# Optimization experiments

Measured on AMD Instinct MI355X. Metric: run time of the kernel, lower is better.

Reference implementation:

```python
import math
import jax, jax.numpy as jnp
import numpy as np

jax.config.update("jax_enable_x64", True)

NUM_HEADS = 4
D_INNER = 256
D_STATE = 256
HEADDIM = D_INNER // NUM_HEADS
NUM_GRAPHS = 8
L_NODES = 512
N_NODES = NUM_GRAPHS * L_NODES
N_EDGES = 65536
TOL = 0.05  # self.tol


def dag_inverse(A, n):
    # Doubling Neumann series: (I+A)(I+A^2)(I+A^4)... = sum_{k<2^ceil(log2 n)} A^k
    # equals (I - A)^{-1} when A is nilpotent (DAG with diameter <= n).
    j = 2 ** math.ceil(math.log2(n))
    I = jnp.eye(A.shape[-1], dtype=A.dtype)
    last = A
    out = I + A
    for _ in range(2, int(math.log2(j)) + 1):
        last = last @ last
        out = out @ (I + last)
    return out


def _forward(x, Bmat, Cmat, dt, dt_edge, dt_bias, D, edge_index, data_batch, diameter):
    Bg, L, H, Hd = NUM_GRAPHS, L_NODES, NUM_HEADS, HEADDIM
    N = x.shape[0]
    # nodes are sorted by graph with equal graph sizes -> local index within graph
    local = jnp.arange(N) - data_batch * L

    def to_dense(v):  # (N, ...) -> (Bg, L, ...), equivalent of to_dense_batch
        return jnp.zeros((Bg, L) + v.shape[1:], v.dtype).at[data_batch, local].set(v)

    x_r = to_dense(x).reshape(Bg, L, H, Hd).transpose(0, 2, 1, 3)  # b n l h
    B_b = jnp.broadcast_to(to_dense(Bmat)[:, None], (Bg, H, L, D_STATE))  # broadcast_bc_in_heads
    C_b = jnp.broadcast_to(to_dense(Cmat)[:, None], (Bg, H, L, D_STATE))

    dt3 = dt.reshape(N, H, 4).transpose(2, 1, 0)  # 'l (n c) -> c n l'
    dt_self_d = to_dense(dt3[3].T).transpose(0, 2, 1)  # (b, n, l)

    def mul_dt_A(d):
        # A_log is a zeros buffer (with_A=False) -> A = -exp(0) = -1
        return -jax.nn.softplus(d + dt_bias[None, :, None])

    dt_A_node = mul_dt_A(dt3[:3])  # (3, n, N)
    dt_A_edge = mul_dt_A(dt_edge.reshape(-1, H, 1).transpose(2, 1, 0))  # (1, n, E)

    src, dst = edge_index[0], edge_index[1]
    dt_A = (dt_A_node[0][:, src] + dt_A_node[1][:, dst] + dt_A_edge[0]) / 3.0  # (n, E)
    vals = jnp.exp(dt_A).T  # (E, n)
    # to_dense_adj: scatter-add edge attrs into dense (b, l1, l2, n)
    adj = jnp.zeros((Bg, L, L, H), vals.dtype).at[
        data_batch[src], local[src], local[dst]].add(vals)
    adj = adj.transpose(0, 3, 1, 2)  # (b, n, l1, l2)

    dt_dummy = to_dense(jnp.exp(dt_A_node[2]).T).transpose(0, 2, 1)  # (b, n, l)
    # normalize_mat('sum_leq', sub_constraint='max')
    normalizer = jnp.maximum(1.0, adj.sum(-1) + dt_dummy)
    A_mat = adj / (normalizer[..., None] + TOL)

    # I_minus_A: fp64 doubling inverse of (I - A^T)
    Lm = dag_inverse(jnp.swapaxes(A_mat.astype(jnp.float64), -1, -2), diameter)
    Lm = Lm.astype(x.dtype)
    L_norm = Lm * dt_self_d[:, :, None, :]  # L * dt_self.unsqueeze(-2)

    y = jnp.einsum('bnld,bnlt,bntd,bnth->bnlh', C_b, L_norm, B_b, x_r)
    y = y + x_r * D[None, :, None, None]
    y = y.transpose(0, 2, 3, 1).reshape(Bg, L, Hd * H)  # 'b n l h -> b l (h n)'
    return y.reshape(N, Hd * H)  # mask is all-True (equal-size graphs)


def setup_inputs():
    key = jax.random.key(0)
    ks = jax.random.split(key, 8)
    x = jax.random.normal(ks[0], (N_NODES, D_INNER), dtype=jnp.float32)
    Bmat = jax.random.normal(ks[1], (N_NODES, D_STATE), dtype=jnp.float32)
    Cmat = jax.random.normal(ks[2], (N_NODES, D_STATE), dtype=jnp.float32)
    dt = jax.random.normal(ks[3], (N_NODES, NUM_HEADS * 4), dtype=jnp.float32)
    dt_edge = jax.random.normal(ks[4], (N_EDGES, NUM_HEADS), dtype=jnp.float32)
    per_graph = N_EDGES // NUM_GRAPHS
    g = jnp.repeat(jnp.arange(NUM_GRAPHS), per_graph)
    src = g * L_NODES + jax.random.randint(ks[5], (N_EDGES,), 0, L_NODES)
    dst = g * L_NODES + jax.random.randint(ks[6], (N_EDGES,), 0, L_NODES)
    edge_index = jnp.stack([src, dst]).astype(jnp.int32)
    data_batch = jnp.repeat(jnp.arange(NUM_GRAPHS), L_NODES).astype(jnp.int32)
    # dt_bias init as in module __init__
    dt_min, dt_max = 1e-3, 1e-1
    u = jax.random.uniform(ks[7], (NUM_HEADS,))
    dtv = jnp.exp(u * (math.log(dt_max) - math.log(dt_min)) + math.log(dt_min))
    dtv = jnp.clip(dtv, 1e-4, None)
    dt_bias = (dtv + jnp.log(-jnp.expm1(-dtv))).astype(jnp.float32)
    D = jnp.ones((NUM_HEADS,), dtype=jnp.float32)
    return {"x": x, "Bmat": Bmat, "Cmat": Cmat, "dt": dt, "dt_edge": dt_edge,
            "dt_bias": dt_bias, "D": D, "edge_index": edge_index,
            "data_batch": data_batch, "diameter": 32}


def reference(x, Bmat, Cmat, dt, dt_edge, dt_bias, D, edge_index, data_batch, diameter):
    return _forward(x, Bmat, Cmat, dt, dt_edge, dt_bias, D, edge_index, data_batch, diameter)
```

## Files before the change

### kernel.cpp

```cpp
#include <hip/hip_runtime.h>
#include <math.h>

#define N_EDGES 65536
#define LNODE 512
#define DSTATE 256
#define DINNER 256
#define HEADD 64

using bf16x8 = __attribute__((ext_vector_type(8))) short;
using f32x4  = __attribute__((ext_vector_type(4))) float;
using us4    = __attribute__((ext_vector_type(4))) unsigned short;
using us8    = __attribute__((ext_vector_type(8))) unsigned short;

__device__ __forceinline__ float softplusf(float z) {
  return (z > 0.0f) ? (z + log1pf(expf(-z))) : log1pf(expf(z));
}
__device__ __forceinline__ float bf2f(unsigned short u) {
  unsigned int x = ((unsigned int)u) << 16;
  return __builtin_bit_cast(float, x);
}
__device__ __forceinline__ unsigned short f2bf(float f) {
  unsigned int x = __builtin_bit_cast(unsigned int, f);
  x += 0x7fffu + ((x >> 16) & 1u);
  return (unsigned short)(x >> 16);
}

__global__ __launch_bounds__(256) void zero_ws_kernel(float* __restrict__ G,
                                                      float* __restrict__ colsum) {
  const size_t i = (size_t)blockIdx.x * 256 + threadIdx.x;
  const float4 z = make_float4(0.0f, 0.0f, 0.0f, 0.0f);
  if (i < 2097152) {
    ((float4*)G)[i] = z;
  } else {
    ((float4*)colsum)[i - 2097152] = z;
  }
}

__global__ void scatter_edges_kernel(const float* __restrict__ dt,
                                     const float* __restrict__ dt_edge,
                                     const float* __restrict__ dt_bias,
                                     const int* __restrict__ edge_index,
                                     float* __restrict__ G,
                                     float* __restrict__ colsum) {
  int t = blockIdx.x * blockDim.x + threadIdx.x;
  if (t >= N_EDGES * 4) return;
  int e = t >> 2;
  int n = t & 3;
  int src = edge_index[e];
  int dst = edge_index[N_EDGES + e];
  float bias = dt_bias[n];
  float z0 = dt[src * 16 + n * 4 + 0] + bias;
  float z1 = dt[dst * 16 + n * 4 + 1] + bias;
  float z2 = dt_edge[e * 4 + n] + bias;
  float val = expf(-(softplusf(z0) + softplusf(z1) + softplusf(z2)) * (1.0f / 3.0f));
  int b = src >> 9;
  int l1 = src & 511;
  int l2 = dst & 511;
  int bn = b * 4 + n;
  atomicAdd(&G[(((size_t)bn) << 18) + ((size_t)l2 << 9) + l1], val);
  atomicAdd(&colsum[bn * 512 + l1], val);
}

__global__ __launch_bounds__(256) void conv_kernel(const float* __restrict__ G,
                                                   const float* __restrict__ colsum,
                                                   const float* __restrict__ dt,
                                                   const float* __restrict__ dt_bias,
                                                   unsigned short* __restrict__ Prm,
                                                   unsigned short* __restrict__ Pt,
                                                   unsigned short* __restrict__ Q) {
  const int bn = blockIdx.y;
  const int n = bn & 3, b = bn >> 2;
  const size_t base = (size_t)bn << 18;
  const int tile = blockIdx.x;
  const int ro = (tile >> 4) << 5;
  const int co = (tile & 15) << 5;
  __shared__ float lds[32][33];
  __shared__ float sinv[32];
  const int t = threadIdx.x;
  if (t < 32) {
    const int col = co + t;
    float ssum = colsum[bn * 512 + col];
    float bias = dt_bias[n];
    float dummy = expf(-softplusf(dt[(size_t)(b * 512 + col) * 16 + n * 4 + 2] + bias));
    float norm = fmaxf(1.0f, ssum + dummy);
    sinv[t] = 1.0f / (norm + 0.05f);
  }
  __syncthreads();
  const int tr = t >> 3;
  const int tc0 = (t & 7) << 2;
  float4 gv = *(const float4*)(G + base + (size_t)(ro + tr) * 512 + co + tc0);
  float vv[4] = {gv.x, gv.y, gv.z, gv.w};
  us4 p, q;
#pragma unroll
  for (int j = 0; j < 4; ++j) {
    vv[j] *= sinv[tc0 + j];
    p[j] = f2bf(vv[j]);
    float qq = vv[j] + (((ro + tr) == (co + tc0 + j)) ? 1.0f : 0.0f);
    q[j] = f2bf(qq);
    lds[tc0 + j][tr] = vv[j];
  }
  *(us4*)(Prm + base + (size_t)(ro + tr) * 512 + co + tc0) = p;
  *(us4*)(Q + base + (size_t)(ro + tr) * 512 + co + tc0) = q;
  __syncthreads();
  us4 pt;
#pragma unroll
  for (int j = 0; j < 4; ++j) pt[j] = f2bf(lds[tr][tc0 + j]);
  *(us4*)(Pt + base + (size_t)(co + tr) * 512 + ro + tc0) = pt;
}

__global__ __launch_bounds__(256) void gemm_pair_kernel(
    const unsigned short* __restrict__ A0, const unsigned short* __restrict__ B0,
    unsigned short* __restrict__ C0rm, unsigned short* __restrict__ C0t,
    const unsigned short* __restrict__ Q0,
    const unsigned short* __restrict__ A1, const unsigned short* __restrict__ B1,
    unsigned short* __restrict__ C1rm, unsigned short* __restrict__ C1t,
    const unsigned short* __restrict__ Q1) {
  const int f = (blockIdx.z * gridDim.y + blockIdx.y) * gridDim.x + blockIdx.x;
  const int rres = f & 7;
  const int q = f >> 3;
  const int tile = q & 15;
  const int kk_ = ((q >> 4) << 3) + rres;
  const int bn = kk_ & 31;
  const int z = kk_ >> 5;

  const unsigned short* A    = z ? A1 : A0;
  const unsigned short* Bt   = z ? B1 : B0;
  unsigned short* Crm        = z ? C1rm : C0rm;
  unsigned short* Ct         = z ? C1t : C0t;
  const unsigned short* Qadd = z ? Q1 : Q0;

  const size_t off = (size_t)bn << 18;
  A += off; Bt += off;
  if (Crm) Crm += off;
  if (Ct) Ct += off;
  if (Qadd) Qadd += off;
  const int m0 = (tile >> 2) << 7;
  const int n0 = (tile & 3) << 7;
  __shared__ __align__(16) char lds[34816];
  const int tid = threadIdx.x;
  const int lane = tid & 63;
  const int w = tid >> 6;
  const int wr = w >> 1, wc = w & 1;

  f32x4 acc[4][4];
#pragma unroll
  for (int i = 0; i < 4; ++i)
#pragma unroll
    for (int j = 0; j < 4; ++j) acc[i][j] = (f32x4)(0.0f);

  auto stage = [&](int buf, int k0) {
    char* la = lds + buf * 16384;
    char* lb = la + 8192;
#pragma unroll
    for (int s = 0; s < 2; ++s) {
      const int fid = s * 256 + tid;
      const int r = fid >> 2;
      const int qs = (fid & 3) ^ ((r >> 1) & 3);
      const unsigned short* ga = A + (size_t)(m0 + r) * 512 + k0 + qs * 8;
      __builtin_amdgcn_global_load_lds(
          (const __attribute__((address_space(1))) void*)ga,
          (__attribute__((address_space(3))) void*)(la + s * 4096 + w * 1024 + (lane << 4)),
          16, 0, 0);
      const unsigned short* gb = Bt + (size_t)(n0 + r) * 512 + k0 + qs * 8;
      __builtin_amdgcn_global_load_lds(
          (const __attribute__((address_space(1))) void*)gb,
          (__attribute__((address_space(3))) void*)(lb + s * 4096 + w * 1024 + (lane << 4)),
          16, 0, 0);
    }
  };

  stage(0, 0);

#pragma unroll
  for (int t = 0; t < 16; ++t) {
    const int cur = t & 1;
    if (t < 15) {
      stage(cur ^ 1, (t + 1) * 32);
      asm volatile("s_waitcnt vmcnt(4)" ::: "memory");
    } else {
      asm volatile("s_waitcnt vmcnt(0)" ::: "memory");
    }
    __builtin_amdgcn_s_barrier();
    __builtin_amdgcn_sched_barrier(0);
    char* la = lds + cur * 16384;
    char* lb = la + 8192;
    const int gk = lane >> 4;
    bf16x8 av[4], bv[4];
#pragma unroll
    for (int mi = 0; mi < 4; ++mi) {
      const int r = wr * 64 + mi * 16 + (lane & 15);
      av[mi] = *(const bf16x8*)(la + r * 64 + ((gk ^ ((r >> 1) & 3)) << 4));
    }
#pragma unroll
    for (int ni = 0; ni < 4; ++ni) {
      const int r = wc * 64 + ni * 16 + (lane & 15);
      bv[ni] = *(const bf16x8*)(lb + r * 64 + ((gk ^ ((r >> 1) & 3)) << 4));
    }
#pragma unroll
    for (int mi = 0; mi < 4; ++mi)
#pragma unroll
      for (int ni = 0; ni < 4; ++ni)
        acc[mi][ni] = __builtin_amdgcn_mfma_f32_16x16x32_bf16(av[mi], bv[ni], acc[mi][ni], 0, 0, 0);
    __builtin_amdgcn_sched_barrier(0);
    __builtin_amdgcn_s_barrier();
  }

  const int cl = lane & 15;
  const int rg = (lane >> 4) << 2;
  unsigned short* tl = (unsigned short*)lds;
#pragma unroll
  for (int mi = 0; mi < 4; ++mi) {
#pragma unroll
    for (int ni = 0; ni < 4; ++ni) {
      const int lrow = wr * 64 + mi * 16 + rg;
      const int lcol = wc * 64 + ni * 16 + cl;
      const int gr = m0 + lrow;
      const int gc = n0 + lcol;
      float v0 = acc[mi][ni][0], v1 = acc[mi][ni][1];
      float v2 = acc[mi][ni][2], v3 = acc[mi][ni][3];
      if (Qadd) {
        v0 += bf2f(Qadd[(size_t)(gr + 0) * 512 + gc]);
        v1 += bf2f(Qadd[(size_t)(gr + 1) * 512 + gc]);
        v2 += bf2f(Qadd[(size_t)(gr + 2) * 512 + gc]);
        v3 += bf2f(Qadd[(size_t)(gr + 3) * 512 + gc]);
      }
      unsigned short h0 = f2bf(v0), h1 = f2bf(v1), h2 = f2bf(v2), h3 = f2bf(v3);
      if (Crm) {
        Crm[(size_t)(gr + 0) * 512 + gc] = h0;
        Crm[(size_t)(gr + 1) * 512 + gc] = h1;
        Crm[(size_t)(gr + 2) * 512 + gc] = h2;
        Crm[(size_t)(gr + 3) * 512 + gc] = h3;
      }
      if (Ct) {
        tl[lcol * 136 + lrow + 0] = h0;
        tl[lcol * 136 + lrow + 1] = h1;
        tl[lcol * 136 + lrow + 2] = h2;
        tl[lcol * 136 + lrow + 3] = h3;
      }
    }
  }
  if (Ct) {
    __syncthreads();
    const int c = tid >> 1;
    const int rh = (tid & 1) << 6;
    const unsigned short* srcp = tl + c * 136 + rh;
    unsigned short* dstp = Ct + (size_t)(n0 + c) * 512 + m0 + rh;
#pragma unroll
    for (int u = 0; u < 8; ++u)
      *(us8*)(dstp + u * 8) = *(const us8*)(srcp + u * 8);
  }
}

__global__ __launch_bounds__(256) void gemm_nt_kernel(const float* __restrict__ Cm,
                                                      const float* __restrict__ Bm,
                                                      float* __restrict__ S) {
  const int f = blockIdx.y * gridDim.x + blockIdx.x;
  const int b = f & 7;
  const int tile = f >> 3;
  const float* Ab = Cm + (size_t)b * LNODE * DSTATE;
  const float* Bb = Bm + (size_t)b * LNODE * DSTATE;
  float* Sb = S + ((size_t)b << 18);
  const int m0 = (tile >> 3) << 6;
  const int n0 = (tile & 7) << 6;
  __shared__ float As[16][68];
  __shared__ float Bs[16][68];
  const int tid = threadIdx.x;
  const int tx = tid & 15, ty = tid >> 4;
  const int srow = tid >> 2, skq = tid & 3;
  float acc[4][4] = {};
  for (int k0 = 0; k0 < DSTATE; k0 += 16) {
    float4 a = *(const float4*)(Ab + (size_t)(m0 + srow) * DSTATE + k0 + skq * 4);
    As[skq * 4 + 0][srow] = a.x; As[skq * 4 + 1][srow] = a.y;
    As[skq * 4 + 2][srow] = a.z; As[skq * 4 + 3][srow] = a.w;
    float4 c = *(const float4*)(Bb + (size_t)(n0 + srow) * DSTATE + k0 + skq * 4);
    Bs[skq * 4 + 0][srow] = c.x; Bs[skq * 4 + 1][srow] = c.y;
    Bs[skq * 4 + 2][srow] = c.z; Bs[skq * 4 + 3][srow] = c.w;
    __syncthreads();
#pragma unroll
    for (int k = 0; k < 16; ++k) {
      float av[4], bv[4];
      *(float4*)(av) = *(const float4*)(&As[k][ty * 4]);
      *(float4*)(bv) = *(const float4*)(&Bs[k][tx * 4]);
#pragma unroll
      for (int i = 0; i < 4; ++i)
#pragma unroll
        for (int j = 0; j < 4; ++j)
          acc[i][j] = fmaf(av[i], bv[j], acc[i][j]);
    }
    __syncthreads();
  }
#pragma unroll
  for (int i = 0; i < 4; ++i) {
    float* sp = Sb + (size_t)(m0 + ty * 4 + i) * 512 + n0 + tx * 4;
    *(float4*)sp = make_float4(acc[i][0], acc[i][1], acc[i][2], acc[i][3]);
  }
}

__global__ __launch_bounds__(256) void final_fused_kernel(
    const unsigned short* __restrict__ Lm, const float* __restrict__ S,
    const float* __restrict__ dt, const float* __restrict__ x,
    float* __restrict__ P) {
  const int f = (blockIdx.z * gridDim.y + blockIdx.y) * gridDim.x + blockIdx.x;
  const int rres = f & 7;
  const int q = f >> 3;
  const int sub = q & 15;
  const int bn = ((q >> 4) << 3) + rres;
  const int ltile = sub & 3;
  const int kg = sub >> 2;
  const int n = bn & 3, b = bn >> 2;
  const unsigned short* Lb = Lm + ((size_t)bn << 18);
  const float* Sb = S + ((size_t)b << 18);
  const float* xb = x + (size_t)b * LNODE * DINNER + n * HEADD;
  const int m0 = ltile << 7;
  const int kbase = kg << 7;
  __shared__ float Ms[16][132];
  __shared__ float Xs[16][64];
  __shared__ float dts_all[128];
  const int tid = threadIdx.x;
  const int tx = tid & 15, ty = tid >> 4;
  if (tid < 128)
    dts_all[tid] = dt[(size_t)(b * 512 + kbase + tid) * 16 + n * 4 + 3];
  __syncthreads();
  float acc[8][4] = {};
  for (int kk0 = 0; kk0 < 128; kk0 += 16) {
    const int k0 = kbase + kk0;
#pragma unroll
    for (int s = 0; s < 2; ++s) {
      int fid = tid + s * 256;
      int m = fid >> 2, kq = fid & 3;
      us4 lm = *(const us4*)(Lb + (size_t)(m0 + m) * 512 + k0 + kq * 4);
      float4 sv = *(const float4*)(Sb + (size_t)(m0 + m) * 512 + k0 + kq * 4);
      Ms[kq * 4 + 0][m] = bf2f(lm[0]) * sv.x * dts_all[kk0 + kq * 4 + 0];
      Ms[kq * 4 + 1][m] = bf2f(lm[1]) * sv.y * dts_all[kk0 + kq * 4 + 1];
      Ms[kq * 4 + 2][m] = bf2f(lm[2]) * sv.z * dts_all[kk0 + kq * 4 + 2];
      Ms[kq * 4 + 3][m] = bf2f(lm[3]) * sv.w * dts_all[kk0 + kq * 4 + 3];
    }
    {
      int kk = tid >> 4, hq = tid & 15;
      float4 v = *(const float4*)(xb + (size_t)(k0 + kk) * DINNER + hq * 4);
      *(float4*)(&Xs[kk][hq * 4]) = v;
    }
    __syncthreads();
#pragma unroll
    for (int k = 0; k < 16; ++k) {
      float mv[8], xv[4];
      *(float4*)(mv)     = *(const float4*)(&Ms[k][ty * 8]);
      *(float4*)(mv + 4) = *(const float4*)(&Ms[k][ty * 8 + 4]);
      *(float4*)(xv)     = *(const float4*)(&Xs[k][tx * 4]);
#pragma unroll
      for (int i = 0; i < 8; ++i)
#pragma unroll
        for (int j = 0; j < 4; ++j)
          acc[i][j] = fmaf(mv[i], xv[j], acc[i][j]);
    }
    __syncthreads();
  }
  float* Pb = P + (((size_t)(kg * 32 + bn)) << 15);
#pragma unroll
  for (int i = 0; i < 8; ++i) {
    const int l = m0 + ty * 8 + i;
    *(float4*)(Pb + (size_t)l * 64 + tx * 4) =
        make_float4(acc[i][0], acc[i][1], acc[i][2], acc[i][3]);
  }
}

__global__ __launch_bounds__(256) void reduce_out_kernel(
    const float* __restrict__ P, const float* __restrict__ x,
    const float* __restrict__ Dv, float* __restrict__ out) {
  int t = blockIdx.x * 256 + threadIdx.x;
  int h = t & 63;
  int l = (t >> 6) & 511;
  int b = t >> 15;
  float4 v;
#pragma unroll
  for (int n = 0; n < 4; ++n) {
    int bn = b * 4 + n;
    float s = 0.0f;
#pragma unroll
    for (int kg = 0; kg < 4; ++kg)
      s += P[(((size_t)(kg * 32 + bn)) << 15) + (size_t)l * 64 + h];
    s += x[(size_t)(b * 512 + l) * 256 + n * 64 + h] * Dv[n];
    ((float*)&v)[n] = s;
  }
  *(float4*)(out + (size_t)(b * 512 + l) * 256 + h * 4) = v;
}

extern "C" void kernel_launch(void* const* d_in, const int* in_sizes, int n_in,
                              void* d_out, int out_size, void* d_ws, size_t ws_size,
                              hipStream_t stream) {
  const float* x        = (const float*)d_in[0];
  const float* Bmat     = (const float*)d_in[1];
  const float* Cmat     = (const float*)d_in[2];
  const float* dt       = (const float*)d_in[3];
  const float* dt_edge  = (const float*)d_in[4];
  const float* dt_bias  = (const float*)d_in[5];
  const float* Dv       = (const float*)d_in[6];
  const int* edge_index = (const int*)d_in[7];
  float* out = (float*)d_out;

  char* wsb = (char*)d_ws;
  const size_t SL = 16777216;
  unsigned short* sA = (unsigned short*)(wsb + 0 * SL);
  unsigned short* sB = (unsigned short*)(wsb + 1 * SL);
  unsigned short* sC = (unsigned short*)(wsb + 2 * SL);
  unsigned short* sD = (unsigned short*)(wsb + 3 * SL);
  unsigned short* sE = (unsigned short*)(wsb + 4 * SL);
  unsigned short* sF = (unsigned short*)(wsb + 5 * SL);
  float* G      = (float*)(wsb + 3 * SL);
  float* Sbuf   = (float*)(wsb + 5 * SL);
  float* Pbuf   = (float*)(wsb + 3 * SL);
  float* colsum = (float*)(wsb + 6 * SL);

  zero_ws_kernel<<<8208, 256, 0, stream>>>(G, colsum);
  scatter_edges_kernel<<<1024, 256, 0, stream>>>(dt, dt_edge, dt_bias, edge_index, G, colsum);
  conv_kernel<<<dim3(256, 32), 256, 0, stream>>>(G, colsum, dt, dt_bias, sA, sB, sC);

  dim3 g1(16, 32, 1), g2(16, 32, 2);
  gemm_pair_kernel<<<g1, 256, 0, stream>>>(sA, sB, sD, sE, nullptr,
                                           nullptr, nullptr, nullptr, nullptr, nullptr);
  gemm_pair_kernel<<<g2, 256, 0, stream>>>(sD, sE, sA, sB, nullptr,
                                           sC, sE, sF, nullptr, sC);
  gemm_pair_kernel<<<g2, 256, 0, stream>>>(sA, sB, sC, sD, nullptr,
                                           sF, sB, sE, nullptr, sF);
  gemm_nt_kernel<<<dim3(64, 8), 256, 0, stream>>>(Cmat, Bmat, Sbuf);
  gemm_pair_kernel<<<g2, 256, 0, stream>>>(sC, sD, nullptr, sA, nullptr,
                                           sE, sD, sB, nullptr, sE);
  gemm_pair_kernel<<<g1, 256, 0, stream>>>(sB, sA, sC, nullptr, sB,
                                           nullptr, nullptr, nullptr, nullptr, nullptr);

  final_fused_kernel<<<dim3(4, 4, 32), 256, 0, stream>>>(sC, Sbuf, dt, x, Pbuf);
  reduce_out_kernel<<<1024, 256, 0, stream>>>(Pbuf, x, Dv, out);
}
```

Measured before the change: 238.6 us.

## Enlarge batched bf16 GEMM tiles to 256x256 with 8-wave interleaved pipeline

```diff
diff --git a/kernel.cpp b/kernel.cpp
--- a/kernel.cpp
+++ b/kernel.cpp
@@ -108,7 +108,7 @@
   *(us4*)(Pt + base + (size_t)(co + tr) * 512 + ro + tc0) = pt;
 }
 
-__global__ __launch_bounds__(256) void gemm_pair_kernel(
+__global__ __launch_bounds__(512) void gemm_pair_kernel(
     const unsigned short* __restrict__ A0, const unsigned short* __restrict__ B0,
     unsigned short* __restrict__ C0rm, unsigned short* __restrict__ C0t,
     const unsigned short* __restrict__ Q0,
@@ -118,10 +118,10 @@
   const int f = (blockIdx.z * gridDim.y + blockIdx.y) * gridDim.x + blockIdx.x;
   const int rres = f & 7;
   const int q = f >> 3;
-  const int tile = q & 15;
-  const int kk_ = ((q >> 4) << 3) + rres;
-  const int bn = kk_ & 31;
-  const int z = kk_ >> 5;
+  const int tile = q & 3;
+  const int unit = ((q >> 2) << 3) + rres;
+  const int bn = unit & 31;
+  const int z = unit >> 5;
 
   const unsigned short* A    = z ? A1 : A0;
   const unsigned short* Bt   = z ? B1 : B0;
@@ -134,88 +134,117 @@
   if (Crm) Crm += off;
   if (Ct) Ct += off;
   if (Qadd) Qadd += off;
-  const int m0 = (tile >> 2) << 7;
-  const int n0 = (tile & 3) << 7;
-  __shared__ __align__(16) char lds[34816];
+  const int m0 = (tile >> 1) << 8;
+  const int n0 = (tile & 1) << 8;
+
+  __shared__ __align__(16) char lds[131072];
   const int tid = threadIdx.x;
   const int lane = tid & 63;
-  const int w = tid >> 6;
-  const int wr = w >> 1, wc = w & 1;
-
-  f32x4 acc[4][4];
-#pragma unroll
-  for (int i = 0; i < 4; ++i)
+  const int wid = tid >> 6;
+  const int wr = wid >> 2;
+  const int wc = wid & 3;
+  const int cl = lane & 15;
+  const int rg = (lane >> 4) << 2;
+
+  f32x4 acc[8][4];
+#pragma unroll
+  for (int i = 0; i < 8; ++i)
 #pragma unroll
     for (int j = 0; j < 4; ++j) acc[i][j] = (f32x4)(0.0f);
 
-  auto stage = [&](int buf, int k0) {
-    char* la = lds + buf * 16384;
-    char* lb = la + 8192;
+  auto stage = [&](int db, int kt, int p) {
+    const unsigned short* src = (p < 2) ? A : Bt;
+    const int t0 = (p < 2) ? m0 : n0;
+    const int dstbase = db * 65536 + ((p >= 2) ? 32768 : 0) + (p & 1) * 16384;
 #pragma unroll
     for (int s = 0; s < 2; ++s) {
-      const int fid = s * 256 + tid;
-      const int r = fid >> 2;
-      const int qs = (fid & 3) ^ ((r >> 1) & 3);
-      const unsigned short* ga = A + (size_t)(m0 + r) * 512 + k0 + qs * 8;
+      const int c = s * 512 + tid;
+      const int row = c >> 3;
+      const int ks = (c & 7) ^ (row & 7);
+      const unsigned short* g =
+          src + (size_t)(t0 + (p & 1) * 128 + row) * 512 + kt * 64 + (ks << 3);
       __builtin_amdgcn_global_load_lds(
-          (const __attribute__((address_space(1))) void*)ga,
-          (__attribute__((address_space(3))) void*)(la + s * 4096 + w * 1024 + (lane << 4)),
+          (const __attribute__((address_space(1))) void*)g,
+          (__attribute__((address_space(3))) void*)(lds + dstbase + c * 16),
           16, 0, 0);
-      const unsigned short* gb = Bt + (size_t)(n0 + r) * 512 + k0 + qs * 8;
-      __builtin_amdgcn_global_load_lds(
-          (const __attribute__((address_space(1))) void*)gb,
-          (__attribute__((address_space(3))) void*)(lb + s * 4096 + w * 1024 + (lane << 4)),
-          16, 0, 0);
     }
   };
 
-  stage(0, 0);
-
-#pragma unroll
-  for (int t = 0; t < 16; ++t) {
-    const int cur = t & 1;
-    if (t < 15) {
-      stage(cur ^ 1, (t + 1) * 32);
-      asm volatile("s_waitcnt vmcnt(4)" ::: "memory");
-    } else {
-      asm volatile("s_waitcnt vmcnt(0)" ::: "memory");
-    }
+  bf16x8 av[4][2];
+  bf16x8 bv[4][2];
+
+  auto readA = [&](int db, int mh) {
+#pragma unroll
+    for (int i = 0; i < 4; ++i)
+#pragma unroll
+      for (int kk = 0; kk < 2; ++kk) {
+        const int row = wr * 128 + (mh * 4 + i) * 16 + cl;
+        int byte = db * 65536 + row * 128 + kk * 64 + ((lane >> 4) << 4);
+        byte ^= (row & 7) << 4;
+        av[i][kk] = *(const bf16x8*)(lds + byte);
+      }
+  };
+  auto readB = [&](int db, int nh) {
+#pragma unroll
+    for (int j = 0; j < 2; ++j)
+#pragma unroll
+      for (int kk = 0; kk < 2; ++kk) {
+        const int ni = nh * 2 + j;
+        const int row = wc * 64 + ni * 16 + cl;
+        int byte = db * 65536 + 32768 + row * 128 + kk * 64 + ((lane >> 4) << 4);
+        byte ^= (row & 7) << 4;
+        bv[ni][kk] = *(const bf16x8*)(lds + byte);
+      }
+  };
+  auto quad = [&](int mh, int nh) {
+    __builtin_amdgcn_s_setprio(1);
+#pragma unroll
+    for (int i = 0; i < 4; ++i)
+#pragma unroll
+      for (int j = 0; j < 2; ++j)
+#pragma unroll
+        for (int kk = 0; kk < 2; ++kk)
+          acc[mh * 4 + i][nh * 2 + j] = __builtin_amdgcn_mfma_f32_16x16x32_bf16(
+              av[i][kk], bv[nh * 2 + j][kk], acc[mh * 4 + i][nh * 2 + j], 0, 0, 0);
+    __builtin_amdgcn_s_setprio(0);
+  };
+
+  stage(0, 0, 0); stage(0, 0, 1); stage(0, 0, 2); stage(0, 0, 3);
+
+#pragma unroll
+  for (int kt = 0; kt < 8; ++kt) {
+    const int d = kt & 1;
+    asm volatile("s_waitcnt vmcnt(0)" ::: "memory");
     __builtin_amdgcn_s_barrier();
     __builtin_amdgcn_sched_barrier(0);
-    char* la = lds + cur * 16384;
-    char* lb = la + 8192;
-    const int gk = lane >> 4;
-    bf16x8 av[4], bv[4];
-#pragma unroll
-    for (int mi = 0; mi < 4; ++mi) {
-      const int r = wr * 64 + mi * 16 + (lane & 15);
-      av[mi] = *(const bf16x8*)(la + r * 64 + ((gk ^ ((r >> 1) & 3)) << 4));
-    }
+    if (kt < 7) stage(d ^ 1, kt + 1, 0);
+    readB(d, 0);
+    readA(d, 0);
+    asm volatile("s_waitcnt lgkmcnt(0)" ::: "memory");
+    __builtin_amdgcn_sched_barrier(0);
+    quad(0, 0);
+    if (kt < 7) stage(d ^ 1, kt + 1, 1);
+    readB(d, 1);
+    asm volatile("s_waitcnt lgkmcnt(0)" ::: "memory");
+    __builtin_amdgcn_sched_barrier(0);
+    quad(0, 1);
+    if (kt < 7) stage(d ^ 1, kt + 1, 2);
+    readA(d, 1);
+    asm volatile("s_waitcnt lgkmcnt(0)" ::: "memory");
+    __builtin_amdgcn_sched_barrier(0);
+    quad(1, 0);
+    if (kt < 7) stage(d ^ 1, kt + 1, 3);
+    quad(1, 1);
+    __builtin_amdgcn_sched_barrier(0);
+  }
+
+  unsigned short hreg[8][4][4];
+#pragma unroll
+  for (int mi = 0; mi < 8; ++mi) {
 #pragma unroll
     for (int ni = 0; ni < 4; ++ni) {
-      const int r = wc * 64 + ni * 16 + (lane & 15);
-      bv[ni] = *(const bf16x8*)(lb + r * 64 + ((gk ^ ((r >> 1) & 3)) << 4));
-    }
-#pragma unroll
-    for (int mi = 0; mi < 4; ++mi)
-#pragma unroll
-      for (int ni = 0; ni < 4; ++ni)
-        acc[mi][ni] = __builtin_amdgcn_mfma_f32_16x16x32_bf16(av[mi], bv[ni], acc[mi][ni], 0, 0, 0);
-    __builtin_amdgcn_sched_barrier(0);
-    __builtin_amdgcn_s_barrier();
-  }
-
-  const int cl = lane & 15;
-  const int rg = (lane >> 4) << 2;
-  unsigned short* tl = (unsigned short*)lds;
-#pragma unroll
-  for (int mi = 0; mi < 4; ++mi) {
-#pragma unroll
-    for (int ni = 0; ni < 4; ++ni) {
-      const int lrow = wr * 64 + mi * 16 + rg;
-      const int lcol = wc * 64 + ni * 16 + cl;
-      const int gr = m0 + lrow;
-      const int gc = n0 + lcol;
+      const int gr = m0 + wr * 128 + mi * 16 + rg;
+      const int gc = n0 + wc * 64 + ni * 16 + cl;
       float v0 = acc[mi][ni][0], v1 = acc[mi][ni][1];
       float v2 = acc[mi][ni][2], v3 = acc[mi][ni][3];
       if (Qadd) {
@@ -225,29 +254,42 @@
         v3 += bf2f(Qadd[(size_t)(gr + 3) * 512 + gc]);
       }
       unsigned short h0 = f2bf(v0), h1 = f2bf(v1), h2 = f2bf(v2), h3 = f2bf(v3);
+      hreg[mi][ni][0] = h0; hreg[mi][ni][1] = h1;
+      hreg[mi][ni][2] = h2; hreg[mi][ni][3] = h3;
       if (Crm) {
         Crm[(size_t)(gr + 0) * 512 + gc] = h0;
         Crm[(size_t)(gr + 1) * 512 + gc] = h1;
         Crm[(size_t)(gr + 2) * 512 + gc] = h2;
         Crm[(size_t)(gr + 3) * 512 + gc] = h3;
       }
-      if (Ct) {
-        tl[lcol * 136 + lrow + 0] = h0;
-        tl[lcol * 136 + lrow + 1] = h1;
-        tl[lcol * 136 + lrow + 2] = h2;
-        tl[lcol * 136 + lrow + 3] = h3;
+    }
+  }
+  if (Ct) {
+    unsigned short* tl = (unsigned short*)lds;
+#pragma unroll
+    for (int p = 0; p < 2; ++p) {
+      __syncthreads();
+      if ((wc >> 1) == p) {
+#pragma unroll
+        for (int mi = 0; mi < 8; ++mi)
+#pragma unroll
+          for (int ni = 0; ni < 4; ++ni) {
+            const int lcol = (wc * 64 + ni * 16 + cl) & 127;
+            const int lrow = wr * 128 + mi * 16 + rg;
+            us4 v; v[0] = hreg[mi][ni][0]; v[1] = hreg[mi][ni][1];
+            v[2] = hreg[mi][ni][2]; v[3] = hreg[mi][ni][3];
+            *(us4*)(tl + lcol * 264 + lrow) = v;
+          }
       }
-    }
-  }
-  if (Ct) {
-    __syncthreads();
-    const int c = tid >> 1;
-    const int rh = (tid & 1) << 6;
-    const unsigned short* srcp = tl + c * 136 + rh;
-    unsigned short* dstp = Ct + (size_t)(n0 + c) * 512 + m0 + rh;
-#pragma unroll
-    for (int u = 0; u < 8; ++u)
-      *(us8*)(dstp + u * 8) = *(const us8*)(srcp + u * 8);
+      __syncthreads();
+      const int c = tid >> 2;
+      const int q4 = tid & 3;
+      const unsigned short* srcp = tl + c * 264 + q4 * 64;
+      unsigned short* dstp = Ct + (size_t)(n0 + p * 128 + c) * 512 + m0 + q4 * 64;
+#pragma unroll
+      for (int u = 0; u < 8; ++u)
+        *(us8*)(dstp + u * 8) = *(const us8*)(srcp + u * 8);
+    }
   }
 }
 
@@ -415,17 +457,17 @@
   scatter_edges_kernel<<<1024, 256, 0, stream>>>(dt, dt_edge, dt_bias, edge_index, G, colsum);
   conv_kernel<<<dim3(256, 32), 256, 0, stream>>>(G, colsum, dt, dt_bias, sA, sB, sC);
 
-  dim3 g1(16, 32, 1), g2(16, 32, 2);
-  gemm_pair_kernel<<<g1, 256, 0, stream>>>(sA, sB, sD, sE, nullptr,
+  dim3 g1(4, 32, 1), g2(4, 32, 2);
+  gemm_pair_kernel<<<g1, 512, 0, stream>>>(sA, sB, sD, sE, nullptr,
                                            nullptr, nullptr, nullptr, nullptr, nullptr);
-  gemm_pair_kernel<<<g2, 256, 0, stream>>>(sD, sE, sA, sB, nullptr,
+  gemm_pair_kernel<<<g2, 512, 0, stream>>>(sD, sE, sA, sB, nullptr,
                                            sC, sE, sF, nullptr, sC);
-  gemm_pair_kernel<<<g2, 256, 0, stream>>>(sA, sB, sC, sD, nullptr,
+  gemm_pair_kernel<<<g2, 512, 0, stream>>>(sA, sB, sC, sD, nullptr,
                                            sF, sB, sE, nullptr, sF);
   gemm_nt_kernel<<<dim3(64, 8), 256, 0, stream>>>(Cmat, Bmat, Sbuf);
-  gemm_pair_kernel<<<g2, 256, 0, stream>>>(sC, sD, nullptr, sA, nullptr,
+  gemm_pair_kernel<<<g2, 512, 0, stream>>>(sC, sD, nullptr, sA, nullptr,
                                            sE, sD, sB, nullptr, sE);
-  gemm_pair_kernel<<<g1, 256, 0, stream>>>(sB, sA, sC, nullptr, sB,
+  gemm_pair_kernel<<<g1, 512, 0, stream>>>(sB, sA, sC, nullptr, sB,
                                            nullptr, nullptr, nullptr, nullptr, nullptr);
 
   final_fused_kernel<<<dim3(4, 4, 32), 256, 0, stream>>>(sC, Sbuf, dt, x, Pbuf);
```

Result: slower. 291.0 us (+21.9%).
